# Performance work log

Hardware: AMD Instinct MI355X
Metric: run time of the kernel (lower is better)

Reference implementation:

```python
import jax, jax.numpy as jnp
import numpy as np

DIM = 2048
DIM_SEQ = 2048
HEADS = 4
BATCH = 4
LN_EPS = 1e-5  # torch nn.LayerNorm default


def setup_inputs() -> dict:
    key = jax.random.key(0)
    k1, k2 = jax.random.split(key)
    init_eps = 0.001 / DIM_SEQ
    x = jax.random.normal(k1, (BATCH, DIM_SEQ, DIM), dtype=jnp.float32)
    weight = jax.random.uniform(k2, (HEADS, DIM_SEQ, DIM_SEQ), dtype=jnp.float32,
                                minval=-init_eps, maxval=init_eps)
    bias = jnp.ones((HEADS, DIM_SEQ), dtype=jnp.float32)
    ln_gamma = jnp.ones((DIM // 2,), dtype=jnp.float32)
    ln_beta = jnp.zeros((DIM // 2,), dtype=jnp.float32)
    return {"x": x, "weight": weight, "bias": bias,
            "ln_gamma": ln_gamma, "ln_beta": ln_beta}


def _layernorm(x, gamma, beta):
    mu = jnp.mean(x, axis=-1, keepdims=True)
    var = jnp.mean(jnp.square(x - mu), axis=-1, keepdims=True)
    return (x - mu) * jax.lax.rsqrt(var + LN_EPS) * gamma + beta


def reference(x, weight, bias, ln_gamma, ln_beta):
    b, n, _ = x.shape
    h = HEADS
    res, gate = jnp.split(x, 2, axis=-1)          # each [b, n, dim/2]
    gate = _layernorm(gate, ln_gamma, ln_beta)
    w = weight[:, :n, :n]                          # [h, n, n]
    bi = bias[:, :n]                               # [h, n]
    # causal: zero strictly-upper triangle (output pos m attends n <= m)
    w = w * jnp.tril(jnp.ones((n, n), dtype=w.dtype))
    d = gate.shape[-1] // h
    gate = gate.reshape(b, n, h, d).transpose(0, 2, 1, 3)   # [b, h, n, d]
    gate = jnp.einsum('bhnd,hmn->bhmd', gate, w)
    gate = gate + bi[None, :, :, None]
    gate = gate.transpose(0, 2, 1, 3).reshape(b, n, h * d)  # [b, n, dim/2]
    return gate * res
```

## Files before the change

kernel.cpp:

```cpp
#include <hip/hip_runtime.h>
#include <hip/hip_bf16.h>

constexpr int Bb = 4;
constexpr int Nn = 2048;
constexpr int DX = 2048;
constexpr int GD = 1024;
constexpr int DH = 256;
constexpr int BM = 128, BD = 128, BK = 32;

typedef short short8v __attribute__((ext_vector_type(8)));
typedef float f32x4   __attribute__((ext_vector_type(4)));

static __device__ __forceinline__ short f2bf(float f) {
    return __builtin_bit_cast(short, __float2bfloat16(f));
}

__global__ __launch_bounds__(256) void ln_stats_kernel(const float* __restrict__ x,
                                                       float* __restrict__ mu,
                                                       float* __restrict__ rstd) {
    int t = threadIdx.x;
    int row = blockIdx.x * 4 + (t >> 6);
    int lane = t & 63;
    const float4* xr = reinterpret_cast<const float4*>(x + (size_t)row * DX + GD);
    float s = 0.f, ss = 0.f;
#pragma unroll
    for (int q = 0; q < 4; ++q) {
        float4 v = xr[q * 64 + lane];
        s  += v.x + v.y + v.z + v.w;
        ss += v.x*v.x + v.y*v.y + v.z*v.z + v.w*v.w;
    }
#pragma unroll
    for (int off = 32; off >= 1; off >>= 1) {
        s  += __shfl_down(s,  off, 64);
        ss += __shfl_down(ss, off, 64);
    }
    if (lane == 0) {
        float m   = s * (1.f / GD);
        float var = ss * (1.f / GD) - m * m;
        mu[row]   = m;
        rstd[row] = rsqrtf(var + 1e-5f);
    }
}

__global__ __launch_bounds__(256, 2) void sgu_mfma_kernel(
    const float* __restrict__ x, const float* __restrict__ w,
    const float* __restrict__ bias, const float* __restrict__ gamma,
    const float* __restrict__ beta, const float* __restrict__ mu,
    const float* __restrict__ rstd, float* __restrict__ out)
{
    __shared__ __align__(16) short Ws[2][BM * BK];
    __shared__ __align__(16) short Gs[2][BK * BD];

    const int t  = threadIdx.x;
    const int bx = blockIdx.x;
    const int dc = bx & 1;
    const int h  = (bx >> 1) & 3;
    const int b  = bx >> 3;
    const int y  = blockIdx.y;
    const int mt = (y < 8) ? (15 - 2 * y) : ((y - 8) * 2);
    const int m0 = mt * BM;
    const int cb = h * DH + dc * BD;
    const int nk = 4 * mt + 4;

    const int lane = t & 63;
    const int wv = t >> 6;
    const int wm = wv >> 1, wc = wv & 1;
    const int g  = lane >> 4;
    const int lr = lane & 15;

    const int sw_row = t >> 1;
    const int sw_kh  = t & 1;
    const int sg_k   = t >> 3;
    const int sg_cs  = t & 7;

    const float* xb   = x + (size_t)b * Nn * DX;
    const float* wrow = w + ((size_t)h * Nn + m0 + sw_row) * Nn + sw_kh * 16;
    const float* gsrc = xb + GD + cb + sg_cs * 16;

    float4 gmv[4], btv[4];
#pragma unroll
    for (int q = 0; q < 4; ++q) {
        gmv[q] = *reinterpret_cast<const float4*>(gamma + cb + sg_cs * 16 + q * 4);
        btv[q] = *reinterpret_cast<const float4*>(beta  + cb + sg_cs * 16 + q * 4);
    }

    f32x4 acc[4][4] = {};
    float4 wreg[4], greg[4];
    float muv = 0.f, rsv = 0.f;

    auto LOADT = [&](int kt) {
        const int n0 = kt * BK;
#pragma unroll
        for (int q = 0; q < 4; ++q)
            wreg[q] = *reinterpret_cast<const float4*>(wrow + n0 + q * 4);
        const float* gp = gsrc + (size_t)(n0 + sg_k) * DX;
#pragma unroll
        for (int q = 0; q < 4; ++q)
            greg[q] = *reinterpret_cast<const float4*>(gp + q * 4);
        muv = mu[b * Nn + n0 + sg_k];
        rsv = rstd[b * Nn + n0 + sg_k];
    };

    auto STAGE = [&](int buf, int kt) {
        const int n0 = kt * BK;
        const int m = m0 + sw_row;
        short8v wlo, whi;
#pragma unroll
        for (int q = 0; q < 4; ++q) {
            float vv[4] = {wreg[q].x, wreg[q].y, wreg[q].z, wreg[q].w};
#pragma unroll
            for (int e = 0; e < 4; ++e) {
                int i = q * 4 + e;
                int n = n0 + sw_kh * 16 + i;
                short bfv = f2bf((n <= m) ? vv[e] : 0.f);
                if (i < 8) wlo[i] = bfv; else whi[i - 8] = bfv;
            }
        }
        char* wl = (char*)&Ws[buf][0];
        unsigned wb = (unsigned)(sw_row * 64 + sw_kh * 32);
        unsigned sz = ((unsigned)(sw_row >> 1) & 3u) << 4;
        *reinterpret_cast<short8v*>(wl + ((wb)      ^ sz)) = wlo;
        *reinterpret_cast<short8v*>(wl + ((wb + 16) ^ sz)) = whi;
        short8v glo, ghi;
#pragma unroll
        for (int q = 0; q < 4; ++q) {
            float vv[4] = {greg[q].x, greg[q].y, greg[q].z, greg[q].w};
            float gm[4] = {gmv[q].x, gmv[q].y, gmv[q].z, gmv[q].w};
            float bt[4] = {btv[q].x, btv[q].y, btv[q].z, btv[q].w};
#pragma unroll
            for (int e = 0; e < 4; ++e) {
                int i = q * 4 + e;
                short bfv = f2bf((vv[e] - muv) * rsv * gm[e] + bt[e]);
                if (i < 8) glo[i] = bfv; else ghi[i - 8] = bfv;
            }
        }
        char* glp = (char*)&Gs[buf][0];
        unsigned gb = (unsigned)(sg_k * 256 + sg_cs * 32);
        unsigned gz = ((unsigned)(sg_k >> 3) & 3u) << 5;
        *reinterpret_cast<short8v*>(glp + ((gb)      ^ gz)) = glo;
        *reinterpret_cast<short8v*>(glp + ((gb + 16) ^ gz)) = ghi;
    };

    auto COMPUTE = [&](int buf) {
        const char* wl = (const char*)&Ws[buf][0];
        const char* glp = (const char*)&Gs[buf][0];
        short8v af[4];
#pragma unroll
        for (int fi = 0; fi < 4; ++fi) {
            int row = wm * 64 + fi * 16 + lr;
            unsigned off = (unsigned)(row * 64 + g * 16);
            off ^= ((unsigned)(row >> 1) & 3u) << 4;
            af[fi] = *reinterpret_cast<const short8v*>(wl + off);
        }
        short8v bf[4];
#pragma unroll
        for (int fj = 0; fj < 4; ++fj) {
            int c = wc * 64 + fj * 16 + lr;
#pragma unroll
            for (int j = 0; j < 8; ++j) {
                int row = g * 8 + j;
                unsigned off = (unsigned)(row * 256 + c * 2);
                off ^= ((unsigned)(row >> 3) & 3u) << 5;
                bf[fj][j] = *reinterpret_cast<const short*>(glp + off);
            }
        }
#pragma unroll
        for (int fi = 0; fi < 4; ++fi)
#pragma unroll
            for (int fj = 0; fj < 4; ++fj)
                acc[fi][fj] = __builtin_amdgcn_mfma_f32_16x16x32_bf16(
                    af[fi], bf[fj], acc[fi][fj], 0, 0, 0);
    };

    LOADT(0);
    STAGE(0, 0);
    __syncthreads();
    int cur = 0;
    for (int kt = 0; kt < nk; ++kt) {
        const bool more = (kt + 1 < nk);
        if (more) LOADT(kt + 1);
        COMPUTE(cur);
        if (more) STAGE(cur ^ 1, kt + 1);
        __syncthreads();
        cur ^= 1;
    }

#pragma unroll
    for (int fi = 0; fi < 4; ++fi) {
#pragma unroll
        for (int r = 0; r < 4; ++r) {
            int m = m0 + wm * 64 + fi * 16 + g * 4 + r;
            float bv = bias[h * Nn + m];
            const float* resrow = xb + (size_t)m * DX + cb;
            float* orow = out + ((size_t)b * Nn + m) * GD + cb;
#pragma unroll
            for (int fj = 0; fj < 4; ++fj) {
                int c = wc * 64 + fj * 16 + lr;
                orow[c] = (acc[fi][fj][r] + bv) * resrow[c];
            }
        }
    }
}

extern "C" void kernel_launch(void* const* d_in, const int* in_sizes, int n_in,
                              void* d_out, int out_size, void* d_ws, size_t ws_size,
                              hipStream_t stream) {
    const float* x     = (const float*)d_in[0];
    const float* w     = (const float*)d_in[1];
    const float* bias  = (const float*)d_in[2];
    const float* gamma = (const float*)d_in[3];
    const float* beta  = (const float*)d_in[4];
    float* out  = (float*)d_out;
    float* mu   = (float*)d_ws;
    float* rstd = mu + Bb * Nn;

    ln_stats_kernel<<<Bb * Nn / 4, 256, 0, stream>>>(x, mu, rstd);

    dim3 grid(32, 16, 1);
    sgu_mfma_kernel<<<grid, 256, 0, stream>>>(x, w, bias, gamma, beta, mu, rstd, out);
}
```

Before: 225.8 us.

## Transpose gate tile in LDS for vector B-fragment reads and preload LN stats

Measured after the change: 253.2 us. +12.1%, slower.

```diff
diff --git a/kernel.cpp b/kernel.cpp
--- a/kernel.cpp
+++ b/kernel.cpp
@@ -9,6 +9,7 @@
 constexpr int BM = 128, BD = 128, BK = 32;
 
 typedef short short8v __attribute__((ext_vector_type(8)));
+typedef short short4v __attribute__((ext_vector_type(4)));
 typedef float f32x4   __attribute__((ext_vector_type(4)));
 
 static __device__ __forceinline__ short f2bf(float f) {
@@ -16,8 +17,7 @@
 }
 
 __global__ __launch_bounds__(256) void ln_stats_kernel(const float* __restrict__ x,
-                                                       float* __restrict__ mu,
-                                                       float* __restrict__ rstd) {
+                                                       float2* __restrict__ mr) {
     int t = threadIdx.x;
     int row = blockIdx.x * 4 + (t >> 6);
     int lane = t & 63;
@@ -37,19 +37,19 @@
     if (lane == 0) {
         float m   = s * (1.f / GD);
         float var = ss * (1.f / GD) - m * m;
-        mu[row]   = m;
-        rstd[row] = rsqrtf(var + 1e-5f);
-    }
-}
-
-__global__ __launch_bounds__(256, 2) void sgu_mfma_kernel(
+        mr[row] = make_float2(m, rsqrtf(var + 1e-5f));
+    }
+}
+
+__global__ __launch_bounds__(256, 3) void sgu_mfma_kernel(
     const float* __restrict__ x, const float* __restrict__ w,
     const float* __restrict__ bias, const float* __restrict__ gamma,
-    const float* __restrict__ beta, const float* __restrict__ mu,
-    const float* __restrict__ rstd, float* __restrict__ out)
+    const float* __restrict__ beta, const float2* __restrict__ mr,
+    float* __restrict__ out)
 {
     __shared__ __align__(16) short Ws[2][BM * BK];
-    __shared__ __align__(16) short Gs[2][BK * BD];
+    __shared__ __align__(16) short Gs[2][BD * BK];
+    __shared__ __align__(16) float2 MR[Nn];
 
     const int t  = threadIdx.x;
     const int bx = blockIdx.x;
@@ -70,35 +70,31 @@
 
     const int sw_row = t >> 1;
     const int sw_kh  = t & 1;
-    const int sg_k   = t >> 3;
-    const int sg_cs  = t & 7;
+    const int sg_c4  = (t & 31) * 4;
+    const int sg_k4  = (t >> 5) * 4;
 
     const float* xb   = x + (size_t)b * Nn * DX;
     const float* wrow = w + ((size_t)h * Nn + m0 + sw_row) * Nn + sw_kh * 16;
-    const float* gsrc = xb + GD + cb + sg_cs * 16;
-
-    float4 gmv[4], btv[4];
-#pragma unroll
-    for (int q = 0; q < 4; ++q) {
-        gmv[q] = *reinterpret_cast<const float4*>(gamma + cb + sg_cs * 16 + q * 4);
-        btv[q] = *reinterpret_cast<const float4*>(beta  + cb + sg_cs * 16 + q * 4);
-    }
+    const float* gsrc = xb + GD + cb + sg_c4;
+    const float2* mrb = mr + b * Nn;
+
+    float4 gmv = *reinterpret_cast<const float4*>(gamma + cb + sg_c4);
+    float4 btv = *reinterpret_cast<const float4*>(beta  + cb + sg_c4);
+    const float gmc[4] = {gmv.x, gmv.y, gmv.z, gmv.w};
+    const float btc[4] = {btv.x, btv.y, btv.z, btv.w};
 
     f32x4 acc[4][4] = {};
-    float4 wreg[4], greg[4];
-    float muv = 0.f, rsv = 0.f;
+    float4 wreg[4];
+    float4 greg[4];
 
     auto LOADT = [&](int kt) {
         const int n0 = kt * BK;
 #pragma unroll
         for (int q = 0; q < 4; ++q)
             wreg[q] = *reinterpret_cast<const float4*>(wrow + n0 + q * 4);
-        const float* gp = gsrc + (size_t)(n0 + sg_k) * DX;
-#pragma unroll
-        for (int q = 0; q < 4; ++q)
-            greg[q] = *reinterpret_cast<const float4*>(gp + q * 4);
-        muv = mu[b * Nn + n0 + sg_k];
-        rsv = rstd[b * Nn + n0 + sg_k];
+#pragma unroll
+        for (int j = 0; j < 4; ++j)
+            greg[j] = *reinterpret_cast<const float4*>(gsrc + (size_t)(n0 + sg_k4 + j) * DX);
     };
 
     auto STAGE = [&](int buf, int kt) {
@@ -121,30 +117,36 @@
         unsigned sz = ((unsigned)(sw_row >> 1) & 3u) << 4;
         *reinterpret_cast<short8v*>(wl + ((wb)      ^ sz)) = wlo;
         *reinterpret_cast<short8v*>(wl + ((wb + 16) ^ sz)) = whi;
-        short8v glo, ghi;
-#pragma unroll
-        for (int q = 0; q < 4; ++q) {
-            float vv[4] = {greg[q].x, greg[q].y, greg[q].z, greg[q].w};
-            float gm[4] = {gmv[q].x, gmv[q].y, gmv[q].z, gmv[q].w};
-            float bt[4] = {btv[q].x, btv[q].y, btv[q].z, btv[q].w};
-#pragma unroll
-            for (int e = 0; e < 4; ++e) {
-                int i = q * 4 + e;
-                short bfv = f2bf((vv[e] - muv) * rsv * gm[e] + bt[e]);
-                if (i < 8) glo[i] = bfv; else ghi[i - 8] = bfv;
-            }
-        }
+        float muk[4], rsk[4];
+        {
+            f32x4 p0 = *reinterpret_cast<const f32x4*>(&MR[n0 + sg_k4]);
+            f32x4 p1 = *reinterpret_cast<const f32x4*>(&MR[n0 + sg_k4 + 2]);
+            muk[0] = p0[0]; rsk[0] = p0[1]; muk[1] = p0[2]; rsk[1] = p0[3];
+            muk[2] = p1[0]; rsk[2] = p1[1]; muk[3] = p1[2]; rsk[3] = p1[3];
+        }
+        float gv[4][4];
+        gv[0][0]=greg[0].x; gv[0][1]=greg[0].y; gv[0][2]=greg[0].z; gv[0][3]=greg[0].w;
+        gv[1][0]=greg[1].x; gv[1][1]=greg[1].y; gv[1][2]=greg[1].z; gv[1][3]=greg[1].w;
+        gv[2][0]=greg[2].x; gv[2][1]=greg[2].y; gv[2][2]=greg[2].z; gv[2][3]=greg[2].w;
+        gv[3][0]=greg[3].x; gv[3][1]=greg[3].y; gv[3][2]=greg[3].z; gv[3][3]=greg[3].w;
         char* glp = (char*)&Gs[buf][0];
-        unsigned gb = (unsigned)(sg_k * 256 + sg_cs * 32);
-        unsigned gz = ((unsigned)(sg_k >> 3) & 3u) << 5;
-        *reinterpret_cast<short8v*>(glp + ((gb)      ^ gz)) = glo;
-        *reinterpret_cast<short8v*>(glp + ((gb + 16) ^ gz)) = ghi;
+#pragma unroll
+        for (int cc = 0; cc < 4; ++cc) {
+            short4v pk;
+#pragma unroll
+            for (int j = 0; j < 4; ++j)
+                pk[j] = f2bf((gv[j][cc] - muk[j]) * rsk[j] * gmc[cc] + btc[cc]);
+            int c = sg_c4 + cc;
+            unsigned off = (unsigned)(c * 64 + sg_k4 * 2);
+            off ^= ((unsigned)(c >> 1) & 3u) << 4;
+            *reinterpret_cast<short4v*>(glp + off) = pk;
+        }
     };
 
     auto COMPUTE = [&](int buf) {
-        const char* wl = (const char*)&Ws[buf][0];
+        const char* wl  = (const char*)&Ws[buf][0];
         const char* glp = (const char*)&Gs[buf][0];
-        short8v af[4];
+        short8v af[4], bfr[4];
 #pragma unroll
         for (int fi = 0; fi < 4; ++fi) {
             int row = wm * 64 + fi * 16 + lr;
@@ -152,29 +154,29 @@
             off ^= ((unsigned)(row >> 1) & 3u) << 4;
             af[fi] = *reinterpret_cast<const short8v*>(wl + off);
         }
-        short8v bf[4];
 #pragma unroll
         for (int fj = 0; fj < 4; ++fj) {
             int c = wc * 64 + fj * 16 + lr;
-#pragma unroll
-            for (int j = 0; j < 8; ++j) {
-                int row = g * 8 + j;
-                unsigned off = (unsigned)(row * 256 + c * 2);
-                off ^= ((unsigned)(row >> 3) & 3u) << 5;
-                bf[fj][j] = *reinterpret_cast<const short*>(glp + off);
-            }
+            unsigned off = (unsigned)(c * 64 + g * 16);
+            off ^= ((unsigned)(c >> 1) & 3u) << 4;
+            bfr[fj] = *reinterpret_cast<const short8v*>(glp + off);
         }
 #pragma unroll
         for (int fi = 0; fi < 4; ++fi)
 #pragma unroll
             for (int fj = 0; fj < 4; ++fj)
                 acc[fi][fj] = __builtin_amdgcn_mfma_f32_16x16x32_bf16(
-                    af[fi], bf[fj], acc[fi][fj], 0, 0, 0);
+                    af[fi], bfr[fj], acc[fi][fj], 0, 0, 0);
     };
 
+    const int nstage = nk * BK;
+    for (int i = t; i < nstage; i += 256)
+        MR[i] = mrb[i];
     LOADT(0);
+    __syncthreads();
     STAGE(0, 0);
     __syncthreads();
+
     int cur = 0;
     for (int kt = 0; kt < nk; ++kt) {
         const bool more = (kt + 1 < nk);
@@ -211,11 +213,10 @@
     const float* gamma = (const float*)d_in[3];
     const float* beta  = (const float*)d_in[4];
     float* out  = (float*)d_out;
-    float* mu   = (float*)d_ws;
-    float* rstd = mu + Bb * Nn;
-
-    ln_stats_kernel<<<Bb * Nn / 4, 256, 0, stream>>>(x, mu, rstd);
+    float2* mrw = (float2*)d_ws;
+
+    ln_stats_kernel<<<Bb * Nn / 4, 256, 0, stream>>>(x, mrw);
 
     dim3 grid(32, 16, 1);
-    sgu_mfma_kernel<<<grid, 256, 0, stream>>>(x, w, bias, gamma, beta, mu, rstd, out);
-}
+    sgu_mfma_kernel<<<grid, 256, 0, stream>>>(x, w, bias, gamma, beta, mrw, out);
+}
```
